# Optimization experiments

Hardware: AMD Instinct MI355X
Metric: run time of the kernel (lower is better)

Reference implementation:

```python
import jax, jax.numpy as jnp
import numpy as np
from jax import lax

WIN = 7                      # skimage default win_size
NP_ = WIN * WIN              # pixels per window (2D)
COV_NORM = NP_ / (NP_ - 1)   # sample covariance normalization (use_sample_covariance=True)
K1, K2 = 0.01, 0.03          # skimage defaults


def setup_inputs() -> dict:
    key = jax.random.key(0)
    k1, k2 = jax.random.split(key)
    B, H, W = 64, 512, 512
    predictions = jax.random.uniform(k1, (B, H, W), dtype=jnp.float32)
    labels = jax.random.uniform(k2, (B, H, W), dtype=jnp.float32)
    return {"predictions": predictions, "labels": labels}


def _mean_filter(x):
    # x: [B, 1, H, W] -> valid 7x7 mean filter. Because skimage crops `pad`
    # border pixels before averaging, a VALID convolution reproduces exactly
    # the pixels that survive the crop (reflect padding never enters them).
    kern = jnp.full((1, 1, WIN, WIN), 1.0 / NP_, dtype=x.dtype)
    return lax.conv_general_dilated(x, kern, (1, 1), 'VALID')


def reference(predictions, labels):
    X = predictions[:, None].astype(jnp.float32)  # [B,1,H,W]
    Y = labels[:, None].astype(jnp.float32)

    # per-sample data_range = max(pred,targ) - min(pred,targ)
    dmax = jnp.maximum(X.max(axis=(1, 2, 3)), Y.max(axis=(1, 2, 3)))
    dmin = jnp.minimum(X.min(axis=(1, 2, 3)), Y.min(axis=(1, 2, 3)))
    dr = (dmax - dmin)[:, None, None, None]       # [B,1,1,1]
    C1 = (K1 * dr) ** 2
    C2 = (K2 * dr) ** 2

    ux = _mean_filter(X)
    uy = _mean_filter(Y)
    uxx = _mean_filter(X * X)
    uyy = _mean_filter(Y * Y)
    uxy = _mean_filter(X * Y)

    vx = COV_NORM * (uxx - ux * ux)
    vy = COV_NORM * (uyy - uy * uy)
    vxy = COV_NORM * (uxy - ux * uy)

    S = ((2.0 * ux * uy + C1) * (2.0 * vxy + C2)) / (
        (ux * ux + uy * uy + C1) * (vx + vy + C2))

    mssim = S.mean(axis=(1, 2, 3))  # per-sample SSIM
    return mssim.mean()             # ssim_total / batch_size
```

## Files before the change

### kernel.cpp

```cpp
#include <hip/hip_runtime.h>

#define Hc     512
#define Wc     512
#define OH     506
#define OW     506
#define NPIX   (Hc * Wc)
#define BATCH  64
#define CHUNKS 16

#define CPW    58
#define NCHUNK 9
#define BH     32
#define NBAND  16
#define WPB    4
#define NPART  (BATCH * NBAND * NCHUNK)

__global__ __launch_bounds__(256) void mm_part_kernel(
    const float* __restrict__ X, const float* __restrict__ Y,
    float* __restrict__ part)
{
    int blk = blockIdx.x;
    int b   = blk >> 4;
    int ch  = blk & 15;
    size_t base = (size_t)b * NPIX + (size_t)ch * (NPIX / CHUNKS);
    const float4* x4 = (const float4*)(X + base);
    const float4* y4 = (const float4*)(Y + base);
    const int n4 = (NPIX / CHUNKS) / 4;

    float mn = 1e38f, mx = -1e38f;
    for (int i = threadIdx.x; i < n4; i += 256) {
        float4 a = x4[i];
        float4 c = y4[i];
        mn = fminf(mn, fminf(fminf(a.x, a.y), fminf(a.z, a.w)));
        mx = fmaxf(mx, fmaxf(fmaxf(a.x, a.y), fmaxf(a.z, a.w)));
        mn = fminf(mn, fminf(fminf(c.x, c.y), fminf(c.z, c.w)));
        mx = fmaxf(mx, fmaxf(fmaxf(c.x, c.y), fmaxf(c.z, c.w)));
    }
    #pragma unroll
    for (int off = 1; off < 64; off <<= 1) {
        mn = fminf(mn, __shfl_xor(mn, off, 64));
        mx = fmaxf(mx, __shfl_xor(mx, off, 64));
    }
    __shared__ float smn[4], smx[4];
    int lane = threadIdx.x & 63, wid = threadIdx.x >> 6;
    if (lane == 0) { smn[wid] = mn; smx[wid] = mx; }
    __syncthreads();
    if (threadIdx.x == 0) {
        mn = fminf(fminf(smn[0], smn[1]), fminf(smn[2], smn[3]));
        mx = fmaxf(fmaxf(smx[0], smx[1]), fmaxf(smx[2], smx[3]));
        part[2 * blk]     = mn;
        part[2 * blk + 1] = mx;
    }
}

__device__ __forceinline__ float h7(float v) {
    float t1 = v + __shfl_down(v, 1, 64);
    float t2 = t1 + __shfl_down(t1, 2, 64);
    return t2 + __shfl_down(t1, 4, 64)
              + __shfl_down(v, 6, 64);
}

__global__ __launch_bounds__(256) void ssim_stream_kernel(
    const float* __restrict__ X, const float* __restrict__ Y,
    const float* __restrict__ mmpart, float* __restrict__ part)
{
    const int lane  = threadIdx.x & 63;
    const int wid   = threadIdx.x >> 6;
    const int chunk = blockIdx.x;
    const int band  = blockIdx.y * WPB + wid;
    const int img   = blockIdx.z;

    float mn = 1e38f, mx = -1e38f;
    #pragma unroll
    for (int ch = 0; ch < CHUNKS; ++ch) {
        mn = fminf(mn, mmpart[2 * (img * CHUNKS + ch)]);
        mx = fmaxf(mx, mmpart[2 * (img * CHUNKS + ch) + 1]);
    }
    const float dr = mx - mn;
    const float C1 = (0.01f * dr) * (0.01f * dr);
    const float C2 = (0.03f * dr) * (0.03f * dr);

    const int col = chunk * CPW + lane;
    const int lc  = col < (Wc - 1) ? col : (Wc - 1);
    const int oy0 = band * BH;
    const int nvalid  = (OH - oy0) < BH ? (OH - oy0) : BH;
    const int ngroups = (nvalid + 6) / 7;
    const float vmask = (lane < CPW && col < OW) ? 1.0f : 0.0f;

    const float* px = X + (size_t)img * NPIX + lc;
    const float* py = Y + (size_t)img * NPIX + lc;

    float rx[7], ry[7];
    float Vx = 0.f, Vy = 0.f, Vxy = 0.f, Vss = 0.f;
    #pragma unroll
    for (int k = 0; k < 6; ++k) {
        float xv = px[(size_t)(oy0 + k) * Wc];
        float yv = py[(size_t)(oy0 + k) * Wc];
        rx[k] = xv; ry[k] = yv;
        Vx += xv; Vy += yv; Vxy += xv * yv; Vss += xv * xv + yv * yv;
    }
    rx[6] = 0.f; ry[6] = 0.f;

    const float inv  = 1.0f / 49.0f;
    const float covn = 49.0f / 48.0f;
    float acc = 0.f;

    for (int g = 0; g < ngroups; ++g) {
        #pragma unroll
        for (int k = 0; k < 7; ++k) {
            const int tt = g * 7 + k;
            int ly = oy0 + tt + 6;
            if (ly > Hc - 1) ly = Hc - 1;
            float xv = px[(size_t)ly * Wc];
            float yv = py[(size_t)ly * Wc];
            Vx += xv; Vy += yv; Vxy += xv * yv; Vss += xv * xv + yv * yv;
            if (tt < nvalid) {
                float Wx = h7(Vx), Wy = h7(Vy);
                float Wxy = h7(Vxy), Wss = h7(Vss);
                float ux   = Wx * inv, uy = Wy * inv;
                float uxuy = ux * uy;
                float u2   = ux * ux + uy * uy;
                float vxy  = covn * (Wxy * inv - uxuy);
                float vss  = covn * (Wss * inv - u2);
                float A1   = 2.f * uxuy + C1;
                float A2   = 2.f * vxy + C2;
                float B1   = u2 + C1;
                float B2   = vss + C2;
                float s    = (A1 * A2) * __builtin_amdgcn_rcpf(B1 * B2);
                acc = fmaf(s, vmask, acc);
            }
            float ox = rx[k], oyv = ry[k];
            Vx -= ox; Vy -= oyv; Vxy -= ox * oyv; Vss -= ox * ox + oyv * oyv;
            rx[(k + 6) % 7] = xv; ry[(k + 6) % 7] = yv;
        }
    }

    #pragma unroll
    for (int off = 1; off < 64; off <<= 1)
        acc += __shfl_xor(acc, off, 64);
    if (lane == 0)
        part[((size_t)img * NBAND + band) * NCHUNK + chunk] = acc;
}

__global__ __launch_bounds__(1024) void final_reduce_kernel(
    const float* __restrict__ part, float* __restrict__ out)
{
    __shared__ double sd[1024];
    double s = 0.0;
    for (int i = threadIdx.x; i < NPART; i += 1024)
        s += (double)part[i];
    sd[threadIdx.x] = s;
    __syncthreads();
    for (int off = 512; off > 0; off >>= 1) {
        if (threadIdx.x < off) sd[threadIdx.x] += sd[threadIdx.x + off];
        __syncthreads();
    }
    if (threadIdx.x == 0)
        out[0] = (float)(sd[0] / ((double)BATCH * OH * OW));
}

extern "C" void kernel_launch(void* const* d_in, const int* in_sizes, int n_in,
                              void* d_out, int out_size, void* d_ws, size_t ws_size,
                              hipStream_t stream) {
    const float* X = (const float*)d_in[0];
    const float* Y = (const float*)d_in[1];
    float* out = (float*)d_out;
    float* ws  = (float*)d_ws;

    float* mmpart = ws;
    float* part   = ws + 2048;

    mm_part_kernel<<<BATCH * CHUNKS, 256, 0, stream>>>(X, Y, mmpart);
    dim3 grid(NCHUNK, NBAND / WPB, BATCH);
    ssim_stream_kernel<<<grid, 64 * WPB, 0, stream>>>(X, Y, mmpart, part);
    final_reduce_kernel<<<1, 1024, 0, stream>>>(part, out);
}
```

Measured before the change: 91.18 us.

## Process four columns per lane with float4 loads and shared-shuffle horizontal sums

Each lane now owns four adjacent columns loaded as float4, so a wave covers 256 columns and only three column chunks are needed instead of nine. The horizontal 7-wide box sum reuses a few shuffles across the four outputs, cutting shuffles per output, and the register ring buffer is replaced by re-reading the outgoing row from memory (likely cache hits). Band height halves to 16 and launch bounds request higher occupancy. The costs are extra global/cache reads for the subtracted row and more registers per lane.

```diff
diff --git a/kernel.cpp b/kernel.cpp
--- a/kernel.cpp
+++ b/kernel.cpp
@@ -8,12 +8,11 @@
 #define BATCH  64
 #define CHUNKS 16
 
-#define CPW    58
-#define NCHUNK 9
-#define BH     32
-#define NBAND  16
+#define BH     16
+#define NBAND  32
+#define NW     3
 #define WPB    4
-#define NPART  (BATCH * NBAND * NCHUNK)
+#define NPART  (BATCH * NBAND * NW)
 
 __global__ __launch_bounds__(256) void mm_part_kernel(
     const float* __restrict__ X, const float* __restrict__ Y,
@@ -53,14 +52,7 @@
     }
 }
 
-__device__ __forceinline__ float h7(float v) {
-    float t1 = v + __shfl_down(v, 1, 64);
-    float t2 = t1 + __shfl_down(t1, 2, 64);
-    return t2 + __shfl_down(t1, 4, 64)
-              + __shfl_down(v, 6, 64);
-}
-
-__global__ __launch_bounds__(256) void ssim_stream_kernel(
+__global__ __launch_bounds__(256, 6) void ssim_stream_kernel(
     const float* __restrict__ X, const float* __restrict__ Y,
     const float* __restrict__ mmpart, float* __restrict__ part)
 {
@@ -80,58 +72,111 @@
     const float C1 = (0.01f * dr) * (0.01f * dr);
     const float C2 = (0.03f * dr) * (0.03f * dr);
 
-    const int col = chunk * CPW + lane;
-    const int lc  = col < (Wc - 1) ? col : (Wc - 1);
+    const int cbase  = (chunk == 0) ? 0 : (chunk == 1) ? 248 : 496;
+    const int out_lo = (chunk == 0) ? 0 : (chunk == 1) ? 250 : 498;
+    const int out_hi = (chunk == 0) ? 249 : (chunk == 1) ? 497 : 505;
+
+    const int col0  = cbase + 4 * lane;
+    const int col0c = (col0 < 508) ? col0 : 508;
+    float vm[4];
+    #pragma unroll
+    for (int j = 0; j < 4; ++j) {
+        int oc = col0 + j;
+        vm[j] = (oc >= out_lo && oc <= out_hi) ? 1.0f : 0.0f;
+    }
+
     const int oy0 = band * BH;
-    const int nvalid  = (OH - oy0) < BH ? (OH - oy0) : BH;
-    const int ngroups = (nvalid + 6) / 7;
-    const float vmask = (lane < CPW && col < OW) ? 1.0f : 0.0f;
-
-    const float* px = X + (size_t)img * NPIX + lc;
-    const float* py = Y + (size_t)img * NPIX + lc;
-
-    float rx[7], ry[7];
-    float Vx = 0.f, Vy = 0.f, Vxy = 0.f, Vss = 0.f;
+    const int nvalid = (OH - oy0) < BH ? (OH - oy0) : BH;
+
+    const float* px = X + (size_t)img * NPIX + col0c;
+    const float* py = Y + (size_t)img * NPIX + col0c;
+
+    float Vx[4] = {0,0,0,0}, Vy[4] = {0,0,0,0};
+    float Vxy[4] = {0,0,0,0}, Vss[4] = {0,0,0,0};
+
     #pragma unroll
     for (int k = 0; k < 6; ++k) {
-        float xv = px[(size_t)(oy0 + k) * Wc];
-        float yv = py[(size_t)(oy0 + k) * Wc];
-        rx[k] = xv; ry[k] = yv;
-        Vx += xv; Vy += yv; Vxy += xv * yv; Vss += xv * xv + yv * yv;
-    }
-    rx[6] = 0.f; ry[6] = 0.f;
+        float4 xa = *(const float4*)(px + (size_t)(oy0 + k) * Wc);
+        float4 ya = *(const float4*)(py + (size_t)(oy0 + k) * Wc);
+        const float xs[4] = {xa.x, xa.y, xa.z, xa.w};
+        const float ys[4] = {ya.x, ya.y, ya.z, ya.w};
+        #pragma unroll
+        for (int i = 0; i < 4; ++i) {
+            Vx[i] += xs[i]; Vy[i] += ys[i];
+            Vxy[i] = fmaf(xs[i], ys[i], Vxy[i]);
+            Vss[i] += fmaf(xs[i], xs[i], ys[i] * ys[i]);
+        }
+    }
 
     const float inv  = 1.0f / 49.0f;
     const float covn = 49.0f / 48.0f;
     float acc = 0.f;
 
-    for (int g = 0; g < ngroups; ++g) {
-        #pragma unroll
-        for (int k = 0; k < 7; ++k) {
-            const int tt = g * 7 + k;
-            int ly = oy0 + tt + 6;
-            if (ly > Hc - 1) ly = Hc - 1;
-            float xv = px[(size_t)ly * Wc];
-            float yv = py[(size_t)ly * Wc];
-            Vx += xv; Vy += yv; Vxy += xv * yv; Vss += xv * xv + yv * yv;
-            if (tt < nvalid) {
-                float Wx = h7(Vx), Wy = h7(Vy);
-                float Wxy = h7(Vxy), Wss = h7(Vss);
-                float ux   = Wx * inv, uy = Wy * inv;
-                float uxuy = ux * uy;
-                float u2   = ux * ux + uy * uy;
-                float vxy  = covn * (Wxy * inv - uxuy);
-                float vss  = covn * (Wss * inv - u2);
-                float A1   = 2.f * uxuy + C1;
-                float A2   = 2.f * vxy + C2;
-                float B1   = u2 + C1;
-                float B2   = vss + C2;
-                float s    = (A1 * A2) * __builtin_amdgcn_rcpf(B1 * B2);
-                acc = fmaf(s, vmask, acc);
+    #pragma unroll 2
+    for (int tt = 0; tt < nvalid; ++tt) {
+        float4 xa = *(const float4*)(px + (size_t)(oy0 + tt + 6) * Wc);
+        float4 ya = *(const float4*)(py + (size_t)(oy0 + tt + 6) * Wc);
+        {
+            const float xs[4] = {xa.x, xa.y, xa.z, xa.w};
+            const float ys[4] = {ya.x, ya.y, ya.z, ya.w};
+            #pragma unroll
+            for (int i = 0; i < 4; ++i) {
+                Vx[i] += xs[i]; Vy[i] += ys[i];
+                Vxy[i] = fmaf(xs[i], ys[i], Vxy[i]);
+                Vss[i] += fmaf(xs[i], xs[i], ys[i] * ys[i]);
             }
-            float ox = rx[k], oyv = ry[k];
-            Vx -= ox; Vy -= oyv; Vxy -= ox * oyv; Vss -= ox * ox + oyv * oyv;
-            rx[(k + 6) % 7] = xv; ry[(k + 6) % 7] = yv;
+        }
+
+        #define H7BLOCK(V, S0, S1, S2, S3)                                   \
+        {                                                                    \
+            float n0 = __shfl_down(V[0], 1, 64);                             \
+            float n1 = __shfl_down(V[1], 1, 64);                             \
+            float n2 = __shfl_down(V[2], 1, 64);                             \
+            float n3 = __shfl_down(V[3], 1, 64);                             \
+            float m0 = __shfl_down(V[0], 2, 64);                             \
+            float m1 = __shfl_down(V[1], 2, 64);                             \
+            S0 = ((V[0] + V[1]) + (V[2] + V[3])) + ((n0 + n1) + n2);         \
+            S1 = S0 + n3 - V[0];                                             \
+            S2 = S1 + m0 - V[1];                                             \
+            S3 = S2 + m1 - V[2];                                             \
+        }
+        float Wx0, Wx1, Wx2, Wx3;   H7BLOCK(Vx,  Wx0, Wx1, Wx2, Wx3)
+        float Wy0, Wy1, Wy2, Wy3;   H7BLOCK(Vy,  Wy0, Wy1, Wy2, Wy3)
+        float Wp0, Wp1, Wp2, Wp3;   H7BLOCK(Vxy, Wp0, Wp1, Wp2, Wp3)
+        float Ws0, Ws1, Ws2, Ws3;   H7BLOCK(Vss, Ws0, Ws1, Ws2, Ws3)
+        #undef H7BLOCK
+
+        #define SSIM1(WxJ, WyJ, WpJ, WsJ, J)                                 \
+        {                                                                    \
+            float ux   = WxJ * inv, uy = WyJ * inv;                          \
+            float uxuy = ux * uy;                                            \
+            float u2   = fmaf(ux, ux, uy * uy);                              \
+            float vxy  = covn * (WpJ * inv - uxuy);                          \
+            float vss  = covn * (WsJ * inv - u2);                            \
+            float A1   = fmaf(2.f, uxuy, C1);                                \
+            float A2   = fmaf(2.f, vxy, C2);                                 \
+            float B1   = u2 + C1;                                            \
+            float B2   = vss + C2;                                           \
+            float s    = (A1 * A2) * __builtin_amdgcn_rcpf(B1 * B2);         \
+            acc = fmaf(s, vm[J], acc);                                       \
+        }
+        SSIM1(Wx0, Wy0, Wp0, Ws0, 0)
+        SSIM1(Wx1, Wy1, Wp1, Ws1, 1)
+        SSIM1(Wx2, Wy2, Wp2, Ws2, 2)
+        SSIM1(Wx3, Wy3, Wp3, Ws3, 3)
+        #undef SSIM1
+
+        float4 xo = *(const float4*)(px + (size_t)(oy0 + tt) * Wc);
+        float4 yo = *(const float4*)(py + (size_t)(oy0 + tt) * Wc);
+        {
+            const float xs[4] = {xo.x, xo.y, xo.z, xo.w};
+            const float ys[4] = {yo.x, yo.y, yo.z, yo.w};
+            #pragma unroll
+            for (int i = 0; i < 4; ++i) {
+                Vx[i] -= xs[i]; Vy[i] -= ys[i];
+                Vxy[i] = fmaf(-xs[i], ys[i], Vxy[i]);
+                Vss[i] -= fmaf(xs[i], xs[i], ys[i] * ys[i]);
+            }
         }
     }
 
@@ -139,7 +184,7 @@
     for (int off = 1; off < 64; off <<= 1)
         acc += __shfl_xor(acc, off, 64);
     if (lane == 0)
-        part[((size_t)img * NBAND + band) * NCHUNK + chunk] = acc;
+        part[((size_t)img * NBAND + band) * NW + chunk] = acc;
 }
 
 __global__ __launch_bounds__(1024) void final_reduce_kernel(
@@ -171,7 +216,7 @@
     float* part   = ws + 2048;
 
     mm_part_kernel<<<BATCH * CHUNKS, 256, 0, stream>>>(X, Y, mmpart);
-    dim3 grid(NCHUNK, NBAND / WPB, BATCH);
+    dim3 grid(NW, NBAND / WPB, BATCH);
     ssim_stream_kernel<<<grid, 64 * WPB, 0, stream>>>(X, Y, mmpart, part);
     final_reduce_kernel<<<1, 1024, 0, stream>>>(part, out);
 }
```

Measured after the change: 84.82 us. 7.0% less time.
